# Optimization experiments

Hardware: AMD Instinct MI355X
Metric: run time of the kernel (lower is better)

The kernel has to match this reference:

```python
import jax, jax.numpy as jnp
import numpy as np

N = 50000   # num_nodes
T = 8       # num_time_steps
C = 64      # feature width (num_features == hidden == num_classes == 64, forced by the module's shape constraints)
E = 800000  # num_edges


def temporal_conv(x, edge_index, time_index, W, b, perturb=None):
    """Faithful TemporalAGNNConv.forward: per-timestep masked scatter-add of
    neighbor features, concat over T, linear + relu. Implemented as a single
    fused (t, dst)-bucketed segment reduce instead of T separate propagates.
    Note: self.lin is dead code in the original; self-loop addition in the
    original would crash (time_index length mismatch) so edges are used as-is.
    """
    src, dst = edge_index[0], edge_index[1]
    msgs = x[src]                                   # [E, C] gather
    seg = time_index * N + dst                      # combined (t, node) bucket
    agg = jax.ops.segment_sum(msgs, seg, num_segments=T * N)   # [T*N, C]
    cat = agg.reshape(T, N, C).transpose(1, 0, 2).reshape(N, T * C)  # [N, T*C]
    out = jax.nn.relu(cat @ W + b)                  # temporal_lin + relu
    if perturb is not None:
        out = out + perturb
    return out


def setup_inputs() -> dict:
    key = jax.random.key(0)
    ks = jax.random.split(key, 11)
    x = jax.random.normal(ks[0], (N, C), jnp.float32)
    edge_index = jax.random.randint(ks[1], (2, E), 0, N, dtype=jnp.int32)
    time_index = jax.random.randint(ks[2], (E,), 0, T, dtype=jnp.int32)
    s_t = 1.0 / np.sqrt(T * C).astype(np.float32)
    # temporal_lin weights stored as [in, out] (torch Linear transposed)
    Wt1 = jax.random.uniform(ks[3], (T * C, C), jnp.float32, -s_t, s_t)
    bt1 = jax.random.uniform(ks[4], (C,), jnp.float32, -s_t, s_t)
    Wt2 = jax.random.uniform(ks[5], (T * C, C), jnp.float32, -s_t, s_t)
    bt2 = jax.random.uniform(ks[6], (C,), jnp.float32, -s_t, s_t)
    s_a1 = 1.0 / np.sqrt(C).astype(np.float32)
    Wa1 = jax.random.uniform(ks[7], (C, 128), jnp.float32, -s_a1, s_a1)
    ba1 = jax.random.uniform(ks[8], (128,), jnp.float32, -s_a1, s_a1)
    s_a2 = 1.0 / np.sqrt(128).astype(np.float32)
    Wa2 = jax.random.uniform(ks[9], (128, C), jnp.float32, -s_a2, s_a2)
    ba2 = jax.random.uniform(ks[10], (C,), jnp.float32, -s_a2, s_a2)
    return {"x": x, "edge_index": edge_index, "time_index": time_index,
            "Wt1": Wt1, "bt1": bt1, "Wt2": Wt2, "bt2": bt2,
            "Wa1": Wa1, "ba1": ba1, "Wa2": Wa2, "ba2": ba2}


def reference(x, edge_index, time_index, Wt1, bt1, Wt2, bt2, Wa1, ba1, Wa2, ba2):
    h1 = jax.nn.relu(temporal_conv(x, edge_index, time_index, Wt1, bt1))   # conv1 + relu
    h2 = temporal_conv(h1, edge_index, time_index, Wt2, bt2)               # conv2 (output width C)
    adv = jax.nn.relu(h2 @ Wa1 + ba1) @ Wa2 + ba2                          # adversary MLP -> [N, C]
    out = temporal_conv(x, edge_index, time_index, Wt1, bt1, perturb=adv)  # conv1 again + perturbation
    return out
```

## Files before the change

kernel.cpp:

```cpp
#include <hip/hip_runtime.h>

#define N_NODES 50000
#define C_FEAT  64
#define E_EDGES 800000
#define KEYS    400000
#define NBLK1   391
#define DPB     16
#define NTILES  (N_NODES / DPB)
#define PBLK_X  1563
#define PBLK_W  128
#define PBLK_A  64
#define PBLK_H  782

typedef __attribute__((ext_vector_type(8))) short short8;
typedef __attribute__((ext_vector_type(4))) float f32x4;

__device__ __forceinline__ float bf2f(unsigned short u) {
    union { unsigned int i; float f; } v; v.i = ((unsigned int)u) << 16; return v.f;
}
__device__ __forceinline__ unsigned short f2bf(float f) {
    union { float f; unsigned int i; } v; v.f = f;
    unsigned int r = v.i + 0x7fff + ((v.i >> 16) & 1);
    return (unsigned short)(r >> 16);
}

__global__ __launch_bounds__(256) void prep_hist(const float* __restrict__ x,
                                                 const float* __restrict__ W1,
                                                 const float* __restrict__ W2,
                                                 const float* __restrict__ Wa1,
                                                 const float* __restrict__ Wa2,
                                                 const int* __restrict__ src,
                                                 const int* __restrict__ dst,
                                                 const int* __restrict__ tix,
                                                 unsigned short* __restrict__ xb,
                                                 unsigned short* __restrict__ WT1,
                                                 unsigned short* __restrict__ WT2,
                                                 unsigned short* __restrict__ Wa1T,
                                                 unsigned short* __restrict__ Wa2T,
                                                 int* __restrict__ cnt,
                                                 int2* __restrict__ rec) {
    const int b = blockIdx.x;
    if (b < PBLK_X) {
        int base = (b * 256 + threadIdx.x) * 8;
        if (base < N_NODES * 64) {
            float4 a = *(const float4*)(x + base);
            float4 c = *(const float4*)(x + base + 4);
            short8 o;
            o[0] = (short)f2bf(a.x); o[1] = (short)f2bf(a.y);
            o[2] = (short)f2bf(a.z); o[3] = (short)f2bf(a.w);
            o[4] = (short)f2bf(c.x); o[5] = (short)f2bf(c.y);
            o[6] = (short)f2bf(c.z); o[7] = (short)f2bf(c.w);
            *(short8*)(xb + base) = o;
        }
    } else if (b < PBLK_X + PBLK_W) {
        int i = (b - PBLK_X) * 256 + threadIdx.x;
        int n = i >> 9, k = i & 511;
        WT1[i] = f2bf(W1[k * 64 + n]);
        WT2[i] = f2bf(W2[k * 64 + n]);
    } else if (b < PBLK_X + PBLK_W + PBLK_A) {
        int i = (b - PBLK_X - PBLK_W) * 256 + threadIdx.x;
        if (i < 8192) {
            int n = i >> 6, k = i & 63;
            Wa1T[i] = f2bf(Wa1[k * 128 + n]);
        } else {
            int ii = i - 8192;
            int n = ii >> 7, k = ii & 127;
            Wa2T[ii] = f2bf(Wa2[k * 64 + n]);
        }
    } else {
        int bb = b - PBLK_X - PBLK_W - PBLK_A;
        const int e0 = bb * 1024 + threadIdx.x * 4;
        if (e0 < E_EDGES) {
            int4 d = *(const int4*)(dst + e0);
            int4 t = *(const int4*)(tix + e0);
            int4 s = *(const int4*)(src + e0);
            int dd[4] = {d.x, d.y, d.z, d.w};
            int tt[4] = {t.x, t.y, t.z, t.w};
            int ss[4] = {s.x, s.y, s.z, s.w};
            int rk[4];
            #pragma unroll
            for (int k = 0; k < 4; ++k)
                rk[k] = atomicAdd(&cnt[dd[k] * 8 + tt[k]], 1);
            #pragma unroll
            for (int k = 0; k < 4; ++k)
                rec[e0 + k] = make_int2(ss[k] | (tt[k] << 16) | ((dd[k] & 15) << 19),
                                        (dd[k] * 8 + tt[k]) | (rk[k] << 19));
        }
    }
}

__global__ __launch_bounds__(256) void scan_all(int* __restrict__ cnt,
                                                int* __restrict__ bsum,
                                                int* __restrict__ chunkoff,
                                                int* __restrict__ done) {
    __shared__ int wsum[4];
    __shared__ int ticket;
    const int tid = threadIdx.x;
    const int lane = tid & 63;
    const int wave = tid >> 6;
    const int i4 = blockIdx.x * 256 + tid;
    int4 v = make_int4(0, 0, 0, 0);
    const bool ok = (i4 * 4 < KEYS);
    if (ok) v = ((const int4*)cnt)[i4];
    int s = v.x + v.y + v.z + v.w;
    int sc = s;
    #pragma unroll
    for (int d = 1; d < 64; d <<= 1) {
        int o = __shfl_up(sc, d, 64);
        if (lane >= d) sc += o;
    }
    if (lane == 63) wsum[wave] = sc;
    __syncthreads();
    int wbase = 0;
    #pragma unroll
    for (int w = 0; w < 4; ++w) wbase += (w < wave) ? wsum[w] : 0;
    int base = wbase + sc - s;
    int4 o;
    o.x = base;
    o.y = base + v.x;
    o.z = o.y + v.y;
    o.w = o.z + v.z;
    if (ok) ((int4*)cnt)[i4] = o;
    if (tid == 255) {
        bsum[blockIdx.x] = wbase + sc;
        __threadfence();
        ticket = atomicAdd(done, 1);
    }
    __syncthreads();
    if (ticket == NBLK1 - 1 && wave == 0) {
        int carry = 0;
        #pragma unroll
        for (int g = 0; g < (NBLK1 + 63) / 64; ++g) {
            int j = g * 64 + lane;
            int val = (j < NBLK1) ? atomicAdd(&bsum[j], 0) : 0;
            int scn = val;
            #pragma unroll
            for (int d = 1; d < 64; d <<= 1) {
                int oo = __shfl_up(scn, d, 64);
                if (lane >= d) scn += oo;
            }
            if (j < NBLK1) chunkoff[j] = carry + scn - val;
            carry += __shfl(scn, 63, 64);
        }
    }
}

__global__ __launch_bounds__(256) void scatter_rank(const int2* __restrict__ rec,
                                                    const int* __restrict__ cnt,
                                                    const int* __restrict__ chunkoff,
                                                    int* __restrict__ elist) {
    const int i = (blockIdx.x * 256 + threadIdx.x) * 2;
    if (i < E_EDGES) {
        int4 r = *(const int4*)(rec + i);
        int key0 = r.y & 0x7ffff, rank0 = (int)((unsigned)r.y >> 19);
        int key1 = r.w & 0x7ffff, rank1 = (int)((unsigned)r.w >> 19);
        elist[chunkoff[key0 >> 10] + cnt[key0] + rank0] = r.x;
        elist[chunkoff[key1 >> 10] + cnt[key1] + rank1] = r.z;
    }
}

#define FLUSH(P, V)                                                                   \
    { int _k = (P) >> 16;                                                             \
      if (_k != cur) { scat[cur >> 3][(cur & 7) * 64 + c] = f2bf(acc);                \
                       acc = 0.f; cur = _k; }                                         \
      acc += (V); }

#define EDGE(K)                                                                       \
    int p##K = __builtin_amdgcn_readlane(pv, e + K);                                  \
    float v##K = bf2f(Xb[(size_t)(p##K & 0xffff) * 64 + c]);

template <bool ADV>
__global__ __launch_bounds__(256, 6) void fused_conv(const unsigned short* __restrict__ Xb,
                                                     const unsigned short* __restrict__ WT,
                                                     const float* __restrict__ bias,
                                                     const int* __restrict__ cstart,
                                                     const int* __restrict__ chunkoff,
                                                     const int* __restrict__ elist,
                                                     unsigned short* __restrict__ Hb,
                                                     const unsigned short* __restrict__ Wa1T,
                                                     const float* __restrict__ ba1,
                                                     const unsigned short* __restrict__ Wa2T,
                                                     const float* __restrict__ ba2,
                                                     const unsigned short* __restrict__ h1r,
                                                     float* __restrict__ outF) {
    __shared__ __attribute__((aligned(16))) unsigned short scat[DPB][520];
    unsigned short (*sH)[72]  = (unsigned short(*)[72])&scat[0][0];
    unsigned short (*sT)[136] = (unsigned short(*)[136])((char*)scat + 4096);
    const int lane = threadIdx.x & 63;
    const int wave = threadIdx.x >> 6;
    const int c = lane;
    const int dbase = blockIdx.x * DPB;

    {
        short8 z = {};
        *(short8*)&scat[wave * 4 + 0][lane * 8] = z;
        *(short8*)&scat[wave * 4 + 1][lane * 8] = z;
        *(short8*)&scat[wave * 4 + 2][lane * 8] = z;
        *(short8*)&scat[wave * 4 + 3][lane * 8] = z;
    }

    const int k0 = (dbase + wave * 4) * 8;
    const int k1 = k0 + 32;
    const int sbeg = chunkoff[k0 >> 10] + cstart[k0];
    const int send = (k1 >= KEYS) ? E_EDGES : chunkoff[k1 >> 10] + cstart[k1];
    int pv = (lane < send - sbeg) ? elist[sbeg + lane] : 0;

    {
        int i = sbeg;
        int cur = 0;
        float acc = 0.f;
        if (i < send) cur = __builtin_amdgcn_readlane(pv, 0) >> 16;
        while (i < send) {
            int cnt = send - i; cnt = (cnt > 64) ? 64 : cnt;
            int pvn = 0;
            if (i + 64 < send) pvn = (lane < send - i - 64) ? elist[i + 64 + lane] : 0;
            int e = 0;
            for (; e + 23 < cnt; e += 24) {
                EDGE(0)  EDGE(1)  EDGE(2)  EDGE(3)
                EDGE(4)  EDGE(5)  EDGE(6)  EDGE(7)
                EDGE(8)  EDGE(9)  EDGE(10) EDGE(11)
                EDGE(12) EDGE(13) EDGE(14) EDGE(15)
                EDGE(16) EDGE(17) EDGE(18) EDGE(19)
                EDGE(20) EDGE(21) EDGE(22) EDGE(23)
                FLUSH(p0, v0)   FLUSH(p1, v1)   FLUSH(p2, v2)   FLUSH(p3, v3)
                FLUSH(p4, v4)   FLUSH(p5, v5)   FLUSH(p6, v6)   FLUSH(p7, v7)
                FLUSH(p8, v8)   FLUSH(p9, v9)   FLUSH(p10, v10) FLUSH(p11, v11)
                FLUSH(p12, v12) FLUSH(p13, v13) FLUSH(p14, v14) FLUSH(p15, v15)
                FLUSH(p16, v16) FLUSH(p17, v17) FLUSH(p18, v18) FLUSH(p19, v19)
                FLUSH(p20, v20) FLUSH(p21, v21) FLUSH(p22, v22) FLUSH(p23, v23)
            }
            if (e + 15 < cnt) {
                EDGE(0)  EDGE(1)  EDGE(2)  EDGE(3)
                EDGE(4)  EDGE(5)  EDGE(6)  EDGE(7)
                EDGE(8)  EDGE(9)  EDGE(10) EDGE(11)
                EDGE(12) EDGE(13) EDGE(14) EDGE(15)
                FLUSH(p0, v0)   FLUSH(p1, v1)   FLUSH(p2, v2)   FLUSH(p3, v3)
                FLUSH(p4, v4)   FLUSH(p5, v5)   FLUSH(p6, v6)   FLUSH(p7, v7)
                FLUSH(p8, v8)   FLUSH(p9, v9)   FLUSH(p10, v10) FLUSH(p11, v11)
                FLUSH(p12, v12) FLUSH(p13, v13) FLUSH(p14, v14) FLUSH(p15, v15)
                e += 16;
            }
            if (e + 7 < cnt) {
                EDGE(0) EDGE(1) EDGE(2) EDGE(3) EDGE(4) EDGE(5) EDGE(6) EDGE(7)
                FLUSH(p0, v0) FLUSH(p1, v1) FLUSH(p2, v2) FLUSH(p3, v3)
                FLUSH(p4, v4) FLUSH(p5, v5) FLUSH(p6, v6) FLUSH(p7, v7)
                e += 8;
            }
            if (e + 3 < cnt) {
                EDGE(0) EDGE(1) EDGE(2) EDGE(3)
                FLUSH(p0, v0) FLUSH(p1, v1) FLUSH(p2, v2) FLUSH(p3, v3)
                e += 4;
            }
            if (e + 1 < cnt) {
                EDGE(0) EDGE(1)
                FLUSH(p0, v0) FLUSH(p1, v1)
                e += 2;
            }
            if (e < cnt) {
                EDGE(0)
                FLUSH(p0, v0)
            }
            i += 64;
            pv = pvn;
        }
        if (sbeg < send)
            scat[cur >> 3][(cur & 7) * 64 + c] = f2bf(acc);
    }
    __syncthreads();

    const int m = lane & 15;
    const int quad = lane >> 4;
    f32x4 acc4 = {0.f, 0.f, 0.f, 0.f};
    {
        const int n0 = wave * 16;
        const unsigned short* wrow = WT + (size_t)(n0 + m) * 512;
        #pragma unroll
        for (int kc = 0; kc < 16; ++kc) {
            short8 af = *(const short8*)&scat[m][kc * 32 + quad * 8];
            short8 bf = *(const short8*)(wrow + kc * 32 + quad * 8);
            acc4 = __builtin_amdgcn_mfma_f32_16x16x32_bf16(af, bf, acc4, 0, 0, 0);
        }
    }

    if (!ADV) {
        const int col = wave * 16 + m;
        const float bcol = bias[col];
        #pragma unroll
        for (int r = 0; r < 4; ++r) {
            int node = dbase + quad * 4 + r;
            Hb[(size_t)node * 64 + col] = f2bf(fmaxf(acc4[r] + bcol, 0.f));
        }
    } else {
        __syncthreads();
        {
            const int col = wave * 16 + m;
            const float bcol = bias[col];
            #pragma unroll
            for (int r = 0; r < 4; ++r)
                sH[quad * 4 + r][col] = f2bf(fmaxf(acc4[r] + bcol, 0.f));
        }
        __syncthreads();
        {
            #pragma unroll
            for (int ct = 0; ct < 2; ++ct) {
                f32x4 a1 = {0.f, 0.f, 0.f, 0.f};
                const int col = (wave * 2 + ct) * 16 + m;
                #pragma unroll
                for (int kc = 0; kc < 2; ++kc) {
                    short8 af = *(const short8*)&sH[m][kc * 32 + quad * 8];
                    short8 bf = *(const short8*)(Wa1T + (size_t)col * 64 + kc * 32 + quad * 8);
                    a1 = __builtin_amdgcn_mfma_f32_16x16x32_bf16(af, bf, a1, 0, 0, 0);
                }
                const float b1 = ba1[col];
                #pragma unroll
                for (int r = 0; r < 4; ++r)
                    sT[quad * 4 + r][col] = f2bf(fmaxf(a1[r] + b1, 0.f));
            }
        }
        __syncthreads();
        {
            f32x4 a2 = {0.f, 0.f, 0.f, 0.f};
            const int col = wave * 16 + m;
            #pragma unroll
            for (int kc = 0; kc < 4; ++kc) {
                short8 af = *(const short8*)&sT[m][kc * 32 + quad * 8];
                short8 bf = *(const short8*)(Wa2T + (size_t)col * 128 + kc * 32 + quad * 8);
                a2 = __builtin_amdgcn_mfma_f32_16x16x32_bf16(af, bf, a2, 0, 0, 0);
            }
            const float b2 = ba2[col];
            #pragma unroll
            for (int r = 0; r < 4; ++r) {
                int node = dbase + quad * 4 + r;
                outF[(size_t)node * 64 + col] =
                    a2[r] + b2 + bf2f(h1r[(size_t)node * 64 + col]);
            }
        }
    }
}

extern "C" void kernel_launch(void* const* d_in, const int* in_sizes, int n_in,
                              void* d_out, int out_size, void* d_ws, size_t ws_size,
                              hipStream_t stream) {
    const float* x   = (const float*)d_in[0];
    const int*   ei  = (const int*)d_in[1];
    const int*   tix = (const int*)d_in[2];
    const float* Wt1 = (const float*)d_in[3];
    const float* bt1 = (const float*)d_in[4];
    const float* Wt2 = (const float*)d_in[5];
    const float* bt2 = (const float*)d_in[6];
    const float* Wa1 = (const float*)d_in[7];
    const float* ba1 = (const float*)d_in[8];
    const float* Wa2 = (const float*)d_in[9];
    const float* ba2 = (const float*)d_in[10];
    float* out = (float*)d_out;

    const int* src = ei;
    const int* dst = ei + E_EDGES;

    unsigned short* xb   = (unsigned short*)d_ws;
    unsigned short* h1b  = xb + (size_t)N_NODES * 64;
    unsigned short* h2b  = h1b + (size_t)N_NODES * 64;
    unsigned short* WT1  = h2b + (size_t)N_NODES * 64;
    unsigned short* WT2  = WT1 + 64 * 512;
    unsigned short* Wa1T = WT2 + 64 * 512;
    unsigned short* Wa2T = Wa1T + 8192;
    int* cnt      = (int*)(Wa2T + 8192);
    int* bsum     = cnt + KEYS;
    int* chunkoff = bsum + 512;
    int* done     = chunkoff + 512;
    int* elist    = done + 64;
    int2* rec     = (int2*)(elist + E_EDGES);

    hipMemsetAsync(cnt, 0, (KEYS + 512 + 512 + 64) * sizeof(int), stream);
    prep_hist<<<PBLK_X + PBLK_W + PBLK_A + PBLK_H, 256, 0, stream>>>(
        x, Wt1, Wt2, Wa1, Wa2, src, dst, tix, xb, WT1, WT2, Wa1T, Wa2T, cnt, rec);
    scan_all<<<NBLK1, 256, 0, stream>>>(cnt, bsum, chunkoff, done);
    scatter_rank<<<(E_EDGES / 2 + 255) / 256, 256, 0, stream>>>(rec, cnt, chunkoff, elist);

    fused_conv<false><<<NTILES, 256, 0, stream>>>(
        xb, WT1, bt1, cnt, chunkoff, elist, h1b,
        nullptr, nullptr, nullptr, nullptr, nullptr, nullptr);
    fused_conv<true><<<NTILES, 256, 0, stream>>>(
        h1b, WT2, bt2, cnt, chunkoff, elist, nullptr,
        Wa1T, ba1, Wa2T, ba2, h1b, out);
}
```

Measured before the change: 245.1 us.

## Split each wave into four node quarters with 4-channel vector gathers

Before, each wave walked the edge list of four destination nodes one edge at a time, with each lane loading one bf16 channel. Now each 16-lane quarter of the wave owns one destination node, and each lane loads 4 channels (8 bytes) per edge. Every wave instruction therefore handles edges for four nodes at once. The aim is fewer serialized edge iterations and wider memory loads. The cost is lane divergence when the nodes have unequal degrees, because the loop runs to the largest of the four edge counts and pads the shorter ones with masked work.

```diff
diff --git a/kernel.cpp b/kernel.cpp
--- a/kernel.cpp
+++ b/kernel.cpp
@@ -159,15 +159,25 @@
     }
 }
 
-#define FLUSH(P, V)                                                                   \
-    { int _k = (P) >> 16;                                                             \
-      if (_k != cur) { scat[cur >> 3][(cur & 7) * 64 + c] = f2bf(acc);                \
-                       acc = 0.f; cur = _k; }                                         \
-      acc += (V); }
+#define STORE_ACC                                                                     \
+    { unsigned int o0 = (unsigned)f2bf(acc0) | ((unsigned)f2bf(acc1) << 16);          \
+      unsigned int o1 = (unsigned)f2bf(acc2) | ((unsigned)f2bf(acc3) << 16);          \
+      uint2 ov; ov.x = o0; ov.y = o1;                                                 \
+      *(uint2*)&scat[cur >> 3][((cur & 7) << 6) + (cl << 2)] = ov; }
 
 #define EDGE(K)                                                                       \
-    int p##K = __builtin_amdgcn_readlane(pv, e + K);                                  \
-    float v##K = bf2f(Xb[(size_t)(p##K & 0xffff) * 64 + c]);
+    int p##K = __shfl(pv, bq + (K), 64);                                              \
+    const bool ok##K = (i + (K)) < len;                                               \
+    uint2 u##K = *(const uint2*)(Xb + ((size_t)(unsigned)(ok##K ? (p##K & 0xffff) : 0) << 6) + (cl << 2)); \
+    if (!ok##K) { u##K.x = 0; u##K.y = 0; }
+
+#define FLUSH(K)                                                                      \
+    { int _k = ok##K ? (p##K >> 16) : cur;                                            \
+      if (_k != cur) { STORE_ACC; acc0 = acc1 = acc2 = acc3 = 0.f; cur = _k; }        \
+      acc0 += bf2f((unsigned short)(u##K.x));                                         \
+      acc1 += bf2f((unsigned short)(u##K.x >> 16));                                   \
+      acc2 += bf2f((unsigned short)(u##K.y));                                         \
+      acc3 += bf2f((unsigned short)(u##K.y >> 16)); }
 
 template <bool ADV>
 __global__ __launch_bounds__(256, 6) void fused_conv(const unsigned short* __restrict__ Xb,
@@ -188,7 +198,8 @@
     unsigned short (*sT)[136] = (unsigned short(*)[136])((char*)scat + 4096);
     const int lane = threadIdx.x & 63;
     const int wave = threadIdx.x >> 6;
-    const int c = lane;
+    const int cl = lane & 15;
+    const int bq = lane & 48;
     const int dbase = blockIdx.x * DPB;
 
     {
@@ -199,73 +210,41 @@
         *(short8*)&scat[wave * 4 + 3][lane * 8] = z;
     }
 
-    const int k0 = (dbase + wave * 4) * 8;
-    const int k1 = k0 + 32;
-    const int sbeg = chunkoff[k0 >> 10] + cstart[k0];
-    const int send = (k1 >= KEYS) ? E_EDGES : chunkoff[k1 >> 10] + cstart[k1];
-    int pv = (lane < send - sbeg) ? elist[sbeg + lane] : 0;
-
-    {
-        int i = sbeg;
-        int cur = 0;
-        float acc = 0.f;
-        if (i < send) cur = __builtin_amdgcn_readlane(pv, 0) >> 16;
-        while (i < send) {
-            int cnt = send - i; cnt = (cnt > 64) ? 64 : cnt;
-            int pvn = 0;
-            if (i + 64 < send) pvn = (lane < send - i - 64) ? elist[i + 64 + lane] : 0;
-            int e = 0;
-            for (; e + 23 < cnt; e += 24) {
-                EDGE(0)  EDGE(1)  EDGE(2)  EDGE(3)
-                EDGE(4)  EDGE(5)  EDGE(6)  EDGE(7)
-                EDGE(8)  EDGE(9)  EDGE(10) EDGE(11)
-                EDGE(12) EDGE(13) EDGE(14) EDGE(15)
-                EDGE(16) EDGE(17) EDGE(18) EDGE(19)
-                EDGE(20) EDGE(21) EDGE(22) EDGE(23)
-                FLUSH(p0, v0)   FLUSH(p1, v1)   FLUSH(p2, v2)   FLUSH(p3, v3)
-                FLUSH(p4, v4)   FLUSH(p5, v5)   FLUSH(p6, v6)   FLUSH(p7, v7)
-                FLUSH(p8, v8)   FLUSH(p9, v9)   FLUSH(p10, v10) FLUSH(p11, v11)
-                FLUSH(p12, v12) FLUSH(p13, v13) FLUSH(p14, v14) FLUSH(p15, v15)
-                FLUSH(p16, v16) FLUSH(p17, v17) FLUSH(p18, v18) FLUSH(p19, v19)
-                FLUSH(p20, v20) FLUSH(p21, v21) FLUSH(p22, v22) FLUSH(p23, v23)
-            }
-            if (e + 15 < cnt) {
-                EDGE(0)  EDGE(1)  EDGE(2)  EDGE(3)
-                EDGE(4)  EDGE(5)  EDGE(6)  EDGE(7)
-                EDGE(8)  EDGE(9)  EDGE(10) EDGE(11)
-                EDGE(12) EDGE(13) EDGE(14) EDGE(15)
-                FLUSH(p0, v0)   FLUSH(p1, v1)   FLUSH(p2, v2)   FLUSH(p3, v3)
-                FLUSH(p4, v4)   FLUSH(p5, v5)   FLUSH(p6, v6)   FLUSH(p7, v7)
-                FLUSH(p8, v8)   FLUSH(p9, v9)   FLUSH(p10, v10) FLUSH(p11, v11)
-                FLUSH(p12, v12) FLUSH(p13, v13) FLUSH(p14, v14) FLUSH(p15, v15)
-                e += 16;
-            }
-            if (e + 7 < cnt) {
-                EDGE(0) EDGE(1) EDGE(2) EDGE(3) EDGE(4) EDGE(5) EDGE(6) EDGE(7)
-                FLUSH(p0, v0) FLUSH(p1, v1) FLUSH(p2, v2) FLUSH(p3, v3)
-                FLUSH(p4, v4) FLUSH(p5, v5) FLUSH(p6, v6) FLUSH(p7, v7)
-                e += 8;
-            }
-            if (e + 3 < cnt) {
-                EDGE(0) EDGE(1) EDGE(2) EDGE(3)
-                FLUSH(p0, v0) FLUSH(p1, v1) FLUSH(p2, v2) FLUSH(p3, v3)
-                e += 4;
-            }
-            if (e + 1 < cnt) {
-                EDGE(0) EDGE(1)
-                FLUSH(p0, v0) FLUSH(p1, v1)
-                e += 2;
-            }
-            if (e < cnt) {
-                EDGE(0)
-                FLUSH(p0, v0)
-            }
-            i += 64;
-            pv = pvn;
-        }
-        if (sbeg < send)
-            scat[cur >> 3][(cur & 7) * 64 + c] = f2bf(acc);
-    }
+    const int dq = dbase + wave * 4 + (lane >> 4);
+    const int kq = dq * 8;
+    const int kqe = kq + 8;
+    const int qbeg = chunkoff[kq >> 10] + cstart[kq];
+    const int qend = (kqe >= KEYS) ? E_EDGES : chunkoff[kqe >> 10] + cstart[kqe];
+    const int len = qend - qbeg;
+
+    int l0 = __builtin_amdgcn_readlane(len, 0);
+    int l1 = __builtin_amdgcn_readlane(len, 16);
+    int l2 = __builtin_amdgcn_readlane(len, 32);
+    int l3 = __builtin_amdgcn_readlane(len, 48);
+    const int maxw = max(max(l0, l1), max(l2, l3));
+
+    int pv = (cl < len) ? elist[qbeg + cl] : 0;
+    int cur = 0;
+    float acc0 = 0.f, acc1 = 0.f, acc2 = 0.f, acc3 = 0.f;
+    if (len > 0) cur = __shfl(pv, bq, 64) >> 16;
+
+    for (int i = 0; i < maxw; i += 16) {
+        int pvn = 0;
+        {
+            int nx = i + 16 + cl;
+            if (nx < len) pvn = elist[qbeg + nx];
+        }
+        EDGE(0)  EDGE(1)  EDGE(2)  EDGE(3)
+        EDGE(4)  EDGE(5)  EDGE(6)  EDGE(7)
+        EDGE(8)  EDGE(9)  EDGE(10) EDGE(11)
+        EDGE(12) EDGE(13) EDGE(14) EDGE(15)
+        FLUSH(0)  FLUSH(1)  FLUSH(2)  FLUSH(3)
+        FLUSH(4)  FLUSH(5)  FLUSH(6)  FLUSH(7)
+        FLUSH(8)  FLUSH(9)  FLUSH(10) FLUSH(11)
+        FLUSH(12) FLUSH(13) FLUSH(14) FLUSH(15)
+        pv = pvn;
+    }
+    if (len > 0) STORE_ACC;
     __syncthreads();
 
     const int m = lane & 15;
```

Result: slower. 255.5 us (+4.2%).
